# Kernel optimization log

Measured on AMD Instinct MI355X. Metric: run time of the kernel, lower is better.

Reference implementation:

```python
import jax, jax.numpy as jnp
import numpy as np

B, P, C = 32, 8732, 21
TOP_K = 200
CONF_THRESH = 0.01
NMS_THRESH = 0.45
VAR0, VAR1 = 0.1, 0.2  # VOC PRIOR_BOX VARIANCE


def setup_inputs() -> dict:
    key = jax.random.key(0)
    k1, k2, k3 = jax.random.split(key, 3)
    loc_data = jax.random.normal(k1, (B, P, 4), jnp.float32)
    conf_data = jax.random.uniform(k2, (B, P, C), jnp.float32)
    prior_data = jax.random.uniform(k3, (P, 4), jnp.float32)
    return {"loc_data": loc_data, "conf_data": conf_data, "prior_data": prior_data}


def _decode(loc, priors):
    # priors are (cx, cy, w, h); returns (x1, y1, x2, y2)
    cxcy = priors[:, :2] + loc[:, :2] * VAR0 * priors[:, 2:]
    wh = priors[:, 2:] * jnp.exp(loc[:, 2:] * VAR1)
    x1y1 = cxcy - wh * 0.5
    return jnp.concatenate([x1y1, x1y1 + wh], axis=1)  # [P,4]


def _nms_class(boxes, scores):
    # boxes [P,4], scores [P] -> [TOP_K,5] rows of (score, x1, y1, x2, y2)
    s = jnp.where(scores > CONF_THRESH, scores, -1.0)
    top_s, idx = jax.lax.top_k(s, TOP_K)          # descending scores
    b = boxes[idx]                                 # [K,4]
    valid = top_s > CONF_THRESH
    x1, y1, x2, y2 = b[:, 0], b[:, 1], b[:, 2], b[:, 3]
    area = (x2 - x1) * (y2 - y1)
    # pairwise intersection / IoU [K,K]
    xx1 = jnp.maximum(x1[:, None], x1[None, :])
    yy1 = jnp.maximum(y1[:, None], y1[None, :])
    xx2 = jnp.minimum(x2[:, None], x2[None, :])
    yy2 = jnp.minimum(y2[:, None], y2[None, :])
    inter = jnp.clip(xx2 - xx1, 0.0) * jnp.clip(yy2 - yy1, 0.0)
    union = area[:, None] + area[None, :] - inter
    iou = inter / union
    ar = jnp.arange(TOP_K)

    def step(carry, j):
        kept, suppressed = carry
        is_kept = valid[j] & ~suppressed[j]
        kept = kept.at[j].set(is_kept)
        suppressed = suppressed | (is_kept & (iou[j] > NMS_THRESH) & (ar > j))
        return (kept, suppressed), None

    (kept, _), _ = jax.lax.scan(
        step, (jnp.zeros(TOP_K, bool), jnp.zeros(TOP_K, bool)), ar)
    # compact kept rows to the front (matches output[i, cl, :count] = ...)
    pos = jnp.cumsum(kept) - 1
    safe = jnp.where(kept, pos, TOP_K)
    rows = jnp.concatenate([top_s[:, None], b], axis=1)  # [K,5]
    out = jnp.zeros((TOP_K + 1, 5), rows.dtype).at[safe].set(rows)[:TOP_K]
    return out


def reference(loc_data, conf_data, prior_data):
    def per_image(loc, conf):
        boxes = _decode(loc, prior_data)           # [P,4]
        return jax.vmap(lambda s: _nms_class(boxes, s), in_axes=1)(conf)  # [C,K,5]

    out = jax.vmap(per_image)(loc_data, conf_data)  # [B,C,K,5]
    return out.at[:, 0].set(0.0)  # class 0 (background) is skipped in original
```

## Files before the change

kernel.cpp:

```cpp
#include <hip/hip_runtime.h>
#include <stdint.h>

#define B_ 32
#define P_ 8732
#define PPAD 8736
#define C_ 21
#define TOPK 200
#define TGT 228
#define CONF_T 0.01f
#define NMS_T 0.45f
#define NCH2 35
#define NT 512
#define KV4 5

__device__ __forceinline__ uint32_t f2s(float f) {
    uint32_t u = __float_as_uint(f);
    return (u & 0x80000000u) ? ~u : (u | 0x80000000u);
}
__device__ __forceinline__ float s2f(uint32_t s) {
    uint32_t b = (s & 0x80000000u) ? (s & 0x7FFFFFFFu) : ~s;
    return __uint_as_float(b);
}
__device__ __forceinline__ uint32_t keyof(float v) {
    return f2s((v > CONF_T) ? v : -1.0f);
}

__global__ __launch_bounds__(256) void transpose_keys(const float* __restrict__ conf,
                                                      uint32_t* __restrict__ keys) {
    const int b = blockIdx.x / NCH2;
    const int ch = blockIdx.x % NCH2;
    const int p0 = ch * 256;
    const int n = min(256, P_ - p0);
    const int tid = threadIdx.x;
    __shared__ float tile[256 * C_];
    const float4* src4 = (const float4*)(conf + ((size_t)b * P_ + p0) * C_);
    float4* tile4 = (float4*)tile;
    const int tot4 = (n * C_) >> 2;
    for (int i = tid; i < tot4; i += 256) tile4[i] = src4[i];
    __syncthreads();
    uint32_t* dst = keys + (size_t)b * C_ * PPAD + p0;
    const int pg = tid & 63;
    const int cs = tid >> 6;
    const int ng = n >> 2;
    if (pg < ng) {
        for (int c = cs; c < C_; c += 4) {
            const float* tp = &tile[4 * pg * C_ + c];
            uint4 k;
            k.x = keyof(tp[0 * C_]);
            k.y = keyof(tp[1 * C_]);
            k.z = keyof(tp[2 * C_]);
            k.w = keyof(tp[3 * C_]);
            *(uint4*)(dst + (size_t)c * PPAD + 4 * pg) = k;
        }
    }
    if (ch == NCH2 - 1 && pg == ng) {
        for (int c = cs; c < C_; c += 4)
            *(uint4*)(dst + (size_t)c * PPAD + 4 * pg) = make_uint4(0u, 0u, 0u, 0u);
    }
}

template<bool RAW>
__global__ __launch_bounds__(NT, 6) void detect_kernel(
    const float* __restrict__ loc, const float* __restrict__ prior,
    const uint32_t* __restrict__ keys, const float* __restrict__ conf,
    float* __restrict__ out)
{
    const int task = blockIdx.x;
    const int b = task / C_;
    const int c = task % C_;
    const int tid = threadIdx.x;
    const int lane = tid & 63;
    float* outp = out + (size_t)task * TOPK * 5;

    if (c == 0) {
        for (int e = tid; e < TOPK * 5; e += NT) outp[e] = 0.0f;
        return;
    }

    __shared__ uint64_t cand[256];
    __shared__ float4 bbox[TOPK];
    __shared__ float bs[TOPK];
    __shared__ unsigned long long msk[TOPK * 4];
    __shared__ unsigned long long vmask[4];
    __shared__ int order[TOPK];
    __shared__ int s_cnt, s_nk;
    __shared__ int s_c2[2];

    uint4 kv[KV4];
    if (!RAW) {
        const uint4* kp = (const uint4*)(keys + (size_t)task * PPAD);
        #pragma unroll
        for (int r = 0; r < KV4; ++r) {
            int q = tid + r * NT;
            kv[r] = (q < PPAD / 4) ? kp[q] : make_uint4(0u, 0u, 0u, 0u);
        }
    } else {
        const float* sp = conf + (size_t)b * P_ * C_ + c;
        #pragma unroll
        for (int r = 0; r < KV4; ++r) {
            uint32_t uu[4];
            #pragma unroll
            for (int c4 = 0; c4 < 4; ++c4) {
                int p = (tid + r * NT) * 4 + c4;
                if (p < P_) {
                    float v = sp[(size_t)p * C_];
                    v = (v > CONF_T) ? v : -1.0f;
                    uu[c4] = f2s(v);
                } else uu[c4] = 0u;
            }
            kv[r] = make_uint4(uu[0], uu[1], uu[2], uu[3]);
        }
    }

    if (tid == 0) s_cnt = 0;
    if (tid < 2) s_c2[tid] = 0;
    for (int i2 = tid; i2 < TOPK * 4; i2 += NT) msk[i2] = 0ull;
    __syncthreads();

    uint32_t lo = 0u, hi = 0xFFFFFFFFu;
    uint32_t t = f2s(1.0f - (float)TGT / (float)P_);
    uint32_t vthr = 0u;
    for (int it = 0; ; ++it) {
        const int slot = it & 1;
        int my = 0;
        #pragma unroll
        for (int r = 0; r < KV4; ++r)
            my += (kv[r].x >= t) + (kv[r].y >= t) + (kv[r].z >= t) + (kv[r].w >= t);
        #pragma unroll
        for (int d = 1; d < 64; d <<= 1) my += __shfl_down(my, d);
        if (lane == 0) atomicAdd(&s_c2[slot], my);
        __syncthreads();
        const int cnt = s_c2[slot];
        __syncthreads();
        if (tid == 0) s_c2[slot] = 0;
        if (cnt >= TOPK && cnt <= 256) { vthr = t; break; }
        if (cnt > 256) lo = t; else hi = t;
        if (hi - lo <= 1) { vthr = lo; break; }
        uint32_t tn = 0;
        bool bis = (it >= 8) || (cnt == 0);
        if (!bis) {
            const float sc = s2f(t);
            const float sn = 1.0f - (1.0f - sc) * (float)TGT / (float)cnt;
            tn = f2s(sn);
            if (!(tn > lo && tn < hi)) bis = true;
        }
        if (bis) tn = lo + ((hi - lo) >> 1);
        t = tn;
    }

    #pragma unroll
    for (int r = 0; r < KV4; ++r) {
        const int pb = (tid + r * NT) * 4;
        uint32_t uu[4] = {kv[r].x, kv[r].y, kv[r].z, kv[r].w};
        #pragma unroll
        for (int c4 = 0; c4 < 4; ++c4) {
            uint32_t u = uu[c4];
            if (u >= vthr) {
                int pos = atomicAdd(&s_cnt, 1);
                if (pos < 256) cand[pos] = ((uint64_t)u << 32) | (uint32_t)(~(uint32_t)(pb + c4));
            }
        }
    }
    __syncthreads();
    if (tid < 256 && tid >= s_cnt) cand[tid] = 0ull;
    __syncthreads();

    uint64_t v = (tid < 256) ? cand[tid] : 0ull;
    for (int kk = 2; kk <= 256; kk <<= 1) {
        for (int j = kk >> 1; j > 0; j >>= 1) {
            if (j >= 64) {
                __syncthreads();
                if (tid < 256) cand[tid] = v;
                __syncthreads();
                if (tid < 256) {
                    uint64_t pv = cand[tid ^ j];
                    bool keepmax = (((tid & j) == 0) == ((tid & kk) == 0));
                    v = keepmax ? (v > pv ? v : pv) : (v < pv ? v : pv);
                }
            } else if (tid < 256) {
                uint64_t pv = __shfl_xor(v, j);
                bool keepmax = (((tid & j) == 0) == ((tid & kk) == 0));
                v = keepmax ? (v > pv ? v : pv) : (v < pv ? v : pv);
            }
        }
    }

    float my_sc = -1.0f;
    if (tid < TOPK) {
        uint32_t su = (uint32_t)(v >> 32);
        int p = (int)(~(uint32_t)v);
        my_sc = s2f(su);
        const float4 l4 = *(const float4*)(loc + ((size_t)b * P_ + p) * 4);
        const float4 pr = *(const float4*)(prior + (size_t)p * 4);
        float cx = __fadd_rn(pr.x, __fmul_rn(__fmul_rn(l4.x, 0.1f), pr.z));
        float cy = __fadd_rn(pr.y, __fmul_rn(__fmul_rn(l4.y, 0.1f), pr.w));
        float ew = (float)exp((double)__fmul_rn(l4.z, 0.2f));
        float eh = (float)exp((double)__fmul_rn(l4.w, 0.2f));
        float w  = __fmul_rn(pr.z, ew);
        float h  = __fmul_rn(pr.w, eh);
        float x1 = __fsub_rn(cx, __fmul_rn(w, 0.5f));
        float y1 = __fsub_rn(cy, __fmul_rn(h, 0.5f));
        float x2 = __fadd_rn(x1, w);
        float y2 = __fadd_rn(y1, h);
        bs[tid] = my_sc;
        bbox[tid] = make_float4(x1, y1, x2, y2);
    }
    {
        unsigned long long bm = __ballot(tid < TOPK && my_sc > CONF_T);
        if (lane == 0 && tid < 256) vmask[tid >> 6] = bm;
    }
    __syncthreads();

    if (tid < 500) {
        const int rp = tid / 5;
        const int s  = tid - rp * 5;
        #pragma unroll
        for (int pass = 0; pass < 2; ++pass) {
            const int j  = pass ? (199 - rp) : rp;
            const int i0 = j + 1 + s;
            const float4 bj = bbox[j];
            const float  aj = __fmul_rn(__fsub_rn(bj.z, bj.x), __fsub_rn(bj.w, bj.y));
            for (int i = i0; i < TOPK; i += 5) {
                const float4 bi = bbox[i];
                float xx1 = fmaxf(bj.x, bi.x);
                float yy1 = fmaxf(bj.y, bi.y);
                float xx2 = fminf(bj.z, bi.z);
                float yy2 = fminf(bj.w, bi.w);
                float dx = fmaxf(__fsub_rn(xx2, xx1), 0.0f);
                float dy = fmaxf(__fsub_rn(yy2, yy1), 0.0f);
                float inter = __fmul_rn(dx, dy);
                if (inter > 0.0f) {
                    float ai = __fmul_rn(__fsub_rn(bi.z, bi.x), __fsub_rn(bi.w, bi.y));
                    float uni = __fsub_rn(__fadd_rn(aj, ai), inter);
                    float t45 = __fmul_rn(NMS_T, uni);
                    float mar = __fmul_rn(t45, 1e-6f);
                    bool sup;
                    if (inter > __fadd_rn(t45, mar)) sup = true;
                    else if (inter < __fsub_rn(t45, mar)) sup = false;
                    else sup = (inter / uni > NMS_T);
                    if (sup) atomicOr(&msk[j * 4 + (i >> 6)], 1ull << (i & 63));
                }
            }
        }
    }
    __syncthreads();

    if (tid < 64) {
        const int L = tid;
        auto or_reduce = [&](unsigned long long x) {
            #pragma unroll
            for (int d = 1; d < 64; d <<= 1) x |= __shfl_xor(x, d);
            return x;
        };
        unsigned long long s1 = 0, s2 = 0, s3 = 0;
        int nk = 0;
        #pragma unroll
        for (int w = 0; w < 4; ++w) {
            const int j = (w << 6) | L;
            unsigned long long r0 = 0, r1 = 0, r2 = 0, r3 = 0;
            if (j < TOPK) {
                const unsigned long long* mr = &msk[j * 4];
                r0 = mr[0]; r1 = mr[1]; r2 = mr[2]; r3 = mr[3];
            }
            const unsigned long long rself = (w == 0) ? r0 : (w == 1) ? r1
                                           : (w == 2) ? r2 : r3;
            unsigned long long sw = (w == 0) ? 0ull : (w == 1) ? s1
                                  : (w == 2) ? s2 : s3;
            unsigned long long alive = vmask[w] & ~sw;
            unsigned long long pm = 0;
            while (alive) {
                int jl = __ffsll(alive) - 1;
                if (L == 0) order[nk] = (w << 6) | jl;
                ++nk;
                sw |= __shfl(rself, jl);
                pm |= (1ull << jl);
                alive &= ~(sw | (1ull << jl));
            }
            if (pm) {
                const bool picked = (pm >> L) & 1ull;
                if (w == 0) {
                    s1 |= or_reduce(picked ? r1 : 0ull);
                    s2 |= or_reduce(picked ? r2 : 0ull);
                    s3 |= or_reduce(picked ? r3 : 0ull);
                } else if (w == 1) {
                    s2 |= or_reduce(picked ? r2 : 0ull);
                    s3 |= or_reduce(picked ? r3 : 0ull);
                } else if (w == 2) {
                    s3 |= or_reduce(picked ? r3 : 0ull);
                }
            }
        }
        if (L == 0) s_nk = nk;
    }
    __syncthreads();

    const int nk = s_nk;
    for (int e = tid; e < TOPK * 5; e += NT) {
        int r = e / 5;
        int f = e - r * 5;
        float val = 0.0f;
        if (r < nk) {
            int j = order[r];
            float4 bb = bbox[j];
            val = (f == 0) ? bs[j] : (f == 1) ? bb.x : (f == 2) ? bb.y
                : (f == 3) ? bb.z : bb.w;
        }
        outp[e] = val;
    }
}

extern "C" void kernel_launch(void* const* d_in, const int* in_sizes, int n_in,
                              void* d_out, int out_size, void* d_ws, size_t ws_size,
                              hipStream_t stream) {
    const float* loc   = (const float*)d_in[0];
    const float* conf  = (const float*)d_in[1];
    const float* prior = (const float*)d_in[2];
    float* out = (float*)d_out;

    const size_t need = (size_t)B_ * C_ * PPAD * sizeof(uint32_t);
    if (ws_size >= need) {
        uint32_t* keys = (uint32_t*)d_ws;
        transpose_keys<<<B_ * NCH2, 256, 0, stream>>>(conf, keys);
        detect_kernel<false><<<B_ * C_, NT, 0, stream>>>(loc, prior, keys, conf, out);
    } else {
        detect_kernel<true><<<B_ * C_, NT, 0, stream>>>(loc, prior, nullptr, conf, out);
    }
}
```

Before: 124.4 us.

## Prefilter candidates by fixed threshold in scatter kernel instead of transposing all keys

The first kernel no longer writes the full transposed key array. It compares each score against a fixed threshold sized to keep about 300 of 8732, and appends only passing candidates to per-(image,class) global buckets through atomics. The detect kernel then reads at most 448 candidates per task and runs the threshold refinement over those, instead of loading and scanning all 8732 keys. This cuts global traffic and per-task selection work, but adds a memset launch and atomics, and falls back to the raw path when a bucket count is outside [200,448], which depends on the input score distribution.

```diff
diff --git a/kernel.cpp b/kernel.cpp
--- a/kernel.cpp
+++ b/kernel.cpp
@@ -3,15 +3,17 @@
 
 #define B_ 32
 #define P_ 8732
-#define PPAD 8736
 #define C_ 21
 #define TOPK 200
 #define TGT 228
+#define TGT0 300
+#define CAP 448
 #define CONF_T 0.01f
 #define NMS_T 0.45f
 #define NCH2 35
 #define NT 512
 #define KV4 5
+#define NTASK (B_ * C_)
 
 __device__ __forceinline__ uint32_t f2s(float f) {
     uint32_t u = __float_as_uint(f);
@@ -24,9 +26,13 @@
 __device__ __forceinline__ uint32_t keyof(float v) {
     return f2s((v > CONF_T) ? v : -1.0f);
 }
-
-__global__ __launch_bounds__(256) void transpose_keys(const float* __restrict__ conf,
-                                                      uint32_t* __restrict__ keys) {
+__device__ __forceinline__ uint32_t thr0() {
+    return f2s(1.0f - (float)TGT0 / (float)P_);
+}
+
+__global__ __launch_bounds__(256) void scatter_cands(const float* __restrict__ conf,
+                                                     uint32_t* __restrict__ gcnt,
+                                                     uint64_t* __restrict__ gcand) {
     const int b = blockIdx.x / NCH2;
     const int ch = blockIdx.x % NCH2;
     const int p0 = ch * 256;
@@ -38,32 +44,41 @@
     const int tot4 = (n * C_) >> 2;
     for (int i = tid; i < tot4; i += 256) tile4[i] = src4[i];
     __syncthreads();
-    uint32_t* dst = keys + (size_t)b * C_ * PPAD + p0;
+    const uint32_t T0 = thr0();
     const int pg = tid & 63;
     const int cs = tid >> 6;
     const int ng = n >> 2;
     if (pg < ng) {
-        for (int c = cs; c < C_; c += 4) {
+        for (int c = (cs == 0 ? 4 : cs); c < C_; c += 4) {
             const float* tp = &tile[4 * pg * C_ + c];
-            uint4 k;
-            k.x = keyof(tp[0 * C_]);
-            k.y = keyof(tp[1 * C_]);
-            k.z = keyof(tp[2 * C_]);
-            k.w = keyof(tp[3 * C_]);
-            *(uint4*)(dst + (size_t)c * PPAD + 4 * pg) = k;
-        }
-    }
-    if (ch == NCH2 - 1 && pg == ng) {
-        for (int c = cs; c < C_; c += 4)
-            *(uint4*)(dst + (size_t)c * PPAD + 4 * pg) = make_uint4(0u, 0u, 0u, 0u);
-    }
-}
-
-template<bool RAW>
+            uint32_t kk0 = keyof(tp[0 * C_]);
+            uint32_t kk1 = keyof(tp[1 * C_]);
+            uint32_t kk2 = keyof(tp[2 * C_]);
+            uint32_t kk3 = keyof(tp[3 * C_]);
+            int nq = (kk0 >= T0) + (kk1 >= T0) + (kk2 >= T0) + (kk3 >= T0);
+            if (nq) {
+                uint32_t pos = atomicAdd(&gcnt[b * C_ + c], (uint32_t)nq);
+                uint64_t* dst = gcand + (size_t)(b * C_ + c) * CAP;
+                const int pb = p0 + 4 * pg;
+                uint32_t kk[4] = {kk0, kk1, kk2, kk3};
+                #pragma unroll
+                for (int k = 0; k < 4; ++k) {
+                    if (kk[k] >= T0) {
+                        if (pos < CAP)
+                            dst[pos] = ((uint64_t)kk[k] << 32) | (uint32_t)(~(uint32_t)(pb + k));
+                        ++pos;
+                    }
+                }
+            }
+        }
+    }
+}
+
+template<bool HASWS>
 __global__ __launch_bounds__(NT, 6) void detect_kernel(
     const float* __restrict__ loc, const float* __restrict__ prior,
-    const uint32_t* __restrict__ keys, const float* __restrict__ conf,
-    float* __restrict__ out)
+    const uint32_t* __restrict__ gcnt, const uint64_t* __restrict__ gcand,
+    const float* __restrict__ conf, float* __restrict__ out)
 {
     const int task = blockIdx.x;
     const int b = task / C_;
@@ -86,14 +101,19 @@
     __shared__ int s_cnt, s_nk;
     __shared__ int s_c2[2];
 
+    const uint32_t T0 = thr0();
+    int gc = 0;
+    if (HASWS) gc = (int)gcnt[task];
+    const bool fast = HASWS && gc >= TOPK && gc <= CAP;
+
+    if (tid == 0) s_cnt = 0;
+    if (tid < 2) s_c2[tid] = 0;
+    for (int i2 = tid; i2 < TOPK * 4; i2 += NT) msk[i2] = 0ull;
+
+    uint64_t vcand = 0;
     uint4 kv[KV4];
-    if (!RAW) {
-        const uint4* kp = (const uint4*)(keys + (size_t)task * PPAD);
-        #pragma unroll
-        for (int r = 0; r < KV4; ++r) {
-            int q = tid + r * NT;
-            kv[r] = (q < PPAD / 4) ? kp[q] : make_uint4(0u, 0u, 0u, 0u);
-        }
+    if (fast) {
+        if (tid < gc) vcand = gcand[(size_t)task * CAP + tid];
     } else {
         const float* sp = conf + (size_t)b * P_ * C_ + c;
         #pragma unroll
@@ -111,53 +131,91 @@
             kv[r] = make_uint4(uu[0], uu[1], uu[2], uu[3]);
         }
     }
-
-    if (tid == 0) s_cnt = 0;
-    if (tid < 2) s_c2[tid] = 0;
-    for (int i2 = tid; i2 < TOPK * 4; i2 += NT) msk[i2] = 0ull;
-    __syncthreads();
-
-    uint32_t lo = 0u, hi = 0xFFFFFFFFu;
-    uint32_t t = f2s(1.0f - (float)TGT / (float)P_);
-    uint32_t vthr = 0u;
-    for (int it = 0; ; ++it) {
-        const int slot = it & 1;
-        int my = 0;
+    __syncthreads();
+
+    if (fast) {
+        uint32_t vthr = T0;
+        if (gc > 256) {
+            uint32_t lo = T0, hi = 0xFFFFFFFFu;
+            const uint32_t myk = (uint32_t)(vcand >> 32);
+            uint32_t t;
+            {
+                const float sc = s2f(T0);
+                const float sn = 1.0f - (1.0f - sc) * (float)TGT / (float)gc;
+                t = f2s(sn);
+                if (!(t > lo && t < hi)) t = lo + ((hi - lo) >> 1);
+            }
+            for (int it = 0; ; ++it) {
+                const int slot = it & 1;
+                int my = (tid < gc && myk >= t) ? 1 : 0;
+                #pragma unroll
+                for (int d = 1; d < 64; d <<= 1) my += __shfl_down(my, d);
+                if (lane == 0) atomicAdd(&s_c2[slot], my);
+                __syncthreads();
+                const int cnt = s_c2[slot];
+                __syncthreads();
+                if (tid == 0) s_c2[slot] = 0;
+                if (cnt >= TOPK && cnt <= 256) { vthr = t; break; }
+                if (cnt > 256) lo = t; else hi = t;
+                if (hi - lo <= 1) { vthr = lo; break; }
+                uint32_t tn = 0;
+                bool bis = (it >= 8) || (cnt == 0);
+                if (!bis) {
+                    const float sc = s2f(t);
+                    const float sn = 1.0f - (1.0f - sc) * (float)TGT / (float)cnt;
+                    tn = f2s(sn);
+                    if (!(tn > lo && tn < hi)) bis = true;
+                }
+                if (bis) tn = lo + ((hi - lo) >> 1);
+                t = tn;
+            }
+        }
+        if (tid < gc && (uint32_t)(vcand >> 32) >= vthr) {
+            int pos = atomicAdd(&s_cnt, 1);
+            if (pos < 256) cand[pos] = vcand;
+        }
+    } else {
+        uint32_t lo = 0u, hi = 0xFFFFFFFFu;
+        uint32_t t = f2s(1.0f - (float)TGT / (float)P_);
+        uint32_t vthr = 0u;
+        for (int it = 0; ; ++it) {
+            const int slot = it & 1;
+            int my = 0;
+            #pragma unroll
+            for (int r = 0; r < KV4; ++r)
+                my += (kv[r].x >= t) + (kv[r].y >= t) + (kv[r].z >= t) + (kv[r].w >= t);
+            #pragma unroll
+            for (int d = 1; d < 64; d <<= 1) my += __shfl_down(my, d);
+            if (lane == 0) atomicAdd(&s_c2[slot], my);
+            __syncthreads();
+            const int cnt = s_c2[slot];
+            __syncthreads();
+            if (tid == 0) s_c2[slot] = 0;
+            if (cnt >= TOPK && cnt <= 256) { vthr = t; break; }
+            if (cnt > 256) lo = t; else hi = t;
+            if (hi - lo <= 1) { vthr = lo; break; }
+            uint32_t tn = 0;
+            bool bis = (it >= 8) || (cnt == 0);
+            if (!bis) {
+                const float sc = s2f(t);
+                const float sn = 1.0f - (1.0f - sc) * (float)TGT / (float)cnt;
+                tn = f2s(sn);
+                if (!(tn > lo && tn < hi)) bis = true;
+            }
+            if (bis) tn = lo + ((hi - lo) >> 1);
+            t = tn;
+        }
         #pragma unroll
-        for (int r = 0; r < KV4; ++r)
-            my += (kv[r].x >= t) + (kv[r].y >= t) + (kv[r].z >= t) + (kv[r].w >= t);
-        #pragma unroll
-        for (int d = 1; d < 64; d <<= 1) my += __shfl_down(my, d);
-        if (lane == 0) atomicAdd(&s_c2[slot], my);
-        __syncthreads();
-        const int cnt = s_c2[slot];
-        __syncthreads();
-        if (tid == 0) s_c2[slot] = 0;
-        if (cnt >= TOPK && cnt <= 256) { vthr = t; break; }
-        if (cnt > 256) lo = t; else hi = t;
-        if (hi - lo <= 1) { vthr = lo; break; }
-        uint32_t tn = 0;
-        bool bis = (it >= 8) || (cnt == 0);
-        if (!bis) {
-            const float sc = s2f(t);
-            const float sn = 1.0f - (1.0f - sc) * (float)TGT / (float)cnt;
-            tn = f2s(sn);
-            if (!(tn > lo && tn < hi)) bis = true;
-        }
-        if (bis) tn = lo + ((hi - lo) >> 1);
-        t = tn;
-    }
-
-    #pragma unroll
-    for (int r = 0; r < KV4; ++r) {
-        const int pb = (tid + r * NT) * 4;
-        uint32_t uu[4] = {kv[r].x, kv[r].y, kv[r].z, kv[r].w};
-        #pragma unroll
-        for (int c4 = 0; c4 < 4; ++c4) {
-            uint32_t u = uu[c4];
-            if (u >= vthr) {
-                int pos = atomicAdd(&s_cnt, 1);
-                if (pos < 256) cand[pos] = ((uint64_t)u << 32) | (uint32_t)(~(uint32_t)(pb + c4));
+        for (int r = 0; r < KV4; ++r) {
+            const int pb = (tid + r * NT) * 4;
+            uint32_t uu[4] = {kv[r].x, kv[r].y, kv[r].z, kv[r].w};
+            #pragma unroll
+            for (int c4 = 0; c4 < 4; ++c4) {
+                uint32_t u = uu[c4];
+                if (u >= vthr) {
+                    int pos = atomicAdd(&s_cnt, 1);
+                    if (pos < 256) cand[pos] = ((uint64_t)u << 32) | (uint32_t)(~(uint32_t)(pb + c4));
+                }
             }
         }
     }
@@ -317,12 +375,15 @@
     const float* prior = (const float*)d_in[2];
     float* out = (float*)d_out;
 
-    const size_t need = (size_t)B_ * C_ * PPAD * sizeof(uint32_t);
-    if (ws_size >= need) {
-        uint32_t* keys = (uint32_t*)d_ws;
-        transpose_keys<<<B_ * NCH2, 256, 0, stream>>>(conf, keys);
-        detect_kernel<false><<<B_ * C_, NT, 0, stream>>>(loc, prior, keys, conf, out);
+    const size_t cnt_bytes  = 4096;
+    const size_t cand_bytes = (size_t)NTASK * CAP * sizeof(uint64_t);
+    if (ws_size >= cnt_bytes + cand_bytes) {
+        uint32_t* gcnt  = (uint32_t*)d_ws;
+        uint64_t* gcand = (uint64_t*)((char*)d_ws + cnt_bytes);
+        hipMemsetAsync(gcnt, 0, (size_t)NTASK * sizeof(uint32_t), stream);
+        scatter_cands<<<B_ * NCH2, 256, 0, stream>>>(conf, gcnt, gcand);
+        detect_kernel<true><<<NTASK, NT, 0, stream>>>(loc, prior, gcnt, gcand, conf, out);
     } else {
-        detect_kernel<true><<<B_ * C_, NT, 0, stream>>>(loc, prior, nullptr, conf, out);
-    }
-}
+        detect_kernel<false><<<NTASK, NT, 0, stream>>>(loc, prior, nullptr, nullptr, conf, out);
+    }
+}
```

Result: slower. 210.7 us (+69.4%).
